# Performance work log

Hardware: AMD Instinct MI355X
Metric: run time of the kernel (lower is better)

The kernel has to match this reference:

```python
import jax, jax.numpy as jnp
import numpy as np

SEQ, SUB, B, V = 32, 16, 512, 258
U = SEQ // SUB
Z, CH, CO, DH = 512, 1024, 512, 1024


def _lstm_cell(x, h, c, Wi, Wh, bi, bh):
    # torch gate order: input, forget, cell, output
    g = x @ Wi + h @ Wh + bi + bh  # [B, 4H]
    i, f, gg, o = jnp.split(g, 4, axis=-1)
    c = jax.nn.sigmoid(f) * c + jax.nn.sigmoid(i) * jnp.tanh(gg)
    h = jax.nn.sigmoid(o) * jnp.tanh(c)
    return h, c


def _lstm2(xs, h1_0, p1, p2):
    # xs: [T,B,in]; h1_0: [B,H] layer-1 initial hidden.
    # Layer-2 hidden and both cell states start at zero (initialize_state in torch code).
    z0 = jnp.zeros_like(h1_0)
    def step(carry, x):
        h1, c1, h2, c2 = carry
        h1, c1 = _lstm_cell(x, h1, c1, *p1)
        h2, c2 = _lstm_cell(h1, h2, c2, *p2)
        return (h1, c1, h2, c2), h2
    _, hs = jax.lax.scan(step, (h1_0, z0, z0, z0), xs)
    return hs  # [T,B,H] top-layer hidden states


def setup_inputs() -> dict:
    key = jax.random.key(0)
    ks = iter(jax.random.split(key, 40))
    def w(shape, s=0.05):
        return jax.random.normal(next(ks), shape, dtype=jnp.float32) * s
    return {
        "z": jax.random.normal(next(ks), (B, Z), dtype=jnp.float32),
        "x": jax.random.uniform(next(ks), (SEQ, B, V), dtype=jnp.float32),
        "conductor_input": w((1, B, V)),
        "ci_W": w((Z, CH)), "ci_b": w((CH,)),
        "cW1i": w((V, 4 * CH)), "cW1h": w((CH, 4 * CH)), "cb1i": w((4 * CH,)), "cb1h": w((4 * CH,)),
        "cW2i": w((CH, 4 * CH)), "cW2h": w((CH, 4 * CH)), "cb2i": w((4 * CH,)), "cb2h": w((4 * CH,)),
        "co_W": w((CH, CO)), "co_b": w((CO,)),
        "di_W": w((CO, DH)), "di_b": w((DH,)),
        "dW1i": w((CO + V, 4 * DH)), "dW1h": w((DH, 4 * DH)), "db1i": w((4 * DH,)), "db1h": w((4 * DH,)),
        "dW2i": w((DH, 4 * DH)), "dW2h": w((DH, 4 * DH)), "db2i": w((4 * DH,)), "db2h": w((4 * DH,)),
        "fc_W": w((DH, V)), "fc_b": w((V,)),
    }


def reference(z, x, conductor_input, ci_W, ci_b, cW1i, cW1h, cb1i, cb1h, cW2i, cW2h, cb2i, cb2h, co_W, co_b, di_W, di_b, dW1i, dW1h, db1i, db1h, dW2i, dW2h, db2i, db2h, fc_W, fc_b):
    # --- conductor: 2-layer LSTM over U steps of a learned constant input ---
    h1 = jnp.tanh(z @ ci_W + ci_b)  # [B,CH] layer-1 init hidden
    cin = jnp.broadcast_to(conductor_input, (U, B, V))
    ch = _lstm2(cin, h1, (cW1i, cW1h, cb1i, cb1h), (cW2i, cW2h, cb2i, cb2h))  # [U,B,CH]
    c = ch @ co_W + co_b  # [U,B,CO]
    # --- decoder (teacher forcing): state resets each sub-sequence, so the U
    # segments of length SUB are independent given c -> vmap over segments ---
    sos = jnp.zeros((1, B, V), jnp.float32).at[:, :, 0].set(1.0)
    prev = jnp.concatenate([sos, x[:-1]], axis=0).reshape(U, SUB, B, V)
    cb = jnp.broadcast_to(c[:, None], (U, SUB, B, CO))
    dec_in = jnp.concatenate([cb, prev], axis=-1)  # [U,SUB,B,CO+V]
    def run_seg(xs, cj):
        h1_0 = jnp.tanh(cj @ di_W + di_b)  # [B,DH]
        return _lstm2(xs, h1_0, (dW1i, dW1h, db1i, db1h), (dW2i, dW2h, db2i, db2h))
    hs = jax.vmap(run_seg)(dec_in, c)  # [U,SUB,B,DH]
    logp = jax.nn.log_softmax(hs @ fc_W + fc_b, axis=-1)  # log(softmax(.)) fused
    return logp.reshape(SEQ, B, V).transpose(1, 0, 2)  # [B,SEQ,V]
```

## Files before the change

kernel.cpp:

```cpp
#include <hip/hip_runtime.h>
#include <cstddef>
#include <cstdint>


namespace {

typedef short s8v __attribute__((ext_vector_type(8)));
typedef float f4v __attribute__((ext_vector_type(4)));
typedef unsigned short ushort_t;

__device__ inline unsigned short f2bf(float f) {
    union { float f; unsigned u; } v; v.f = f;
    unsigned r = v.u + 0x7fff + ((v.u >> 16) & 1);
    return (unsigned short)(r >> 16);
}
__device__ inline float bf2f(ushort_t u) {
    union { unsigned u; float f; } v; v.u = ((unsigned)u) << 16; return v.f;
}

#define GLOAD_LDS(gp, lp)                                              \
    __builtin_amdgcn_global_load_lds(                                  \
        (const __attribute__((address_space(1))) void*)(gp),           \
        (__attribute__((address_space(3))) void*)(lp), 16, 0, 0)

__device__ __forceinline__ void gemm_core(
    const ushort_t* __restrict__ A1a, const ushort_t* __restrict__ A1b,
    int lda1, int K1, const ushort_t* __restrict__ B1t,
    const ushort_t* __restrict__ A2, int lda2, int K2,
    const ushort_t* __restrict__ B2t,
    int bm, int bn, ushort_t* lds, f4v acc[2][4])
{
    const int tid = threadIdx.x;
    const int wid = tid >> 6;
    const int lane = tid & 63;

    const int srow = wid * 16 + (lane >> 2);
    const int rl = srow ^ ((srow >> 2) & 1);
    const int cle = (((lane & 3) ^ (rl & 3)) << 3);

    const int n1 = K1 >> 5;
    const int nt = n1 + (K2 >> 5);

    auto stage = [&](int buf, int t) {
        const ushort_t *Aa, *Ab, *Bt;
        int lda, ldb, k0;
        if (t < n1) { Aa = A1a; Ab = A1b; lda = lda1; Bt = B1t; ldb = K1; k0 = t * 32; }
        else        { Aa = A2; Ab = nullptr; lda = lda2; Bt = B2t; ldb = K2; k0 = (t - n1) * 32; }
        const int grow = bm + rl;
        const ushort_t* ap = (Ab != nullptr && grow >= 512)
                                 ? Ab + (size_t)(grow - 512) * lda + k0 + cle
                                 : Aa + (size_t)grow * lda + k0 + cle;
        GLOAD_LDS(ap, lds + buf * 6144 + wid * 512);
        const ushort_t* bp = Bt + (size_t)(bn + rl) * ldb + k0 + cle;
        GLOAD_LDS(bp, lds + buf * 6144 + 2048 + wid * 512);
        GLOAD_LDS(bp + (size_t)64 * ldb, lds + buf * 6144 + 4096 + wid * 512);
    };

    const int wr = wid >> 1, wc = wid & 1;
    const int lrow = lane & 15, lkg = lane >> 4;

    int aoff[2], boff[4];
#pragma unroll
    for (int m = 0; m < 2; ++m) {
        const int r = wr * 32 + m * 16 + lrow;
        aoff[m] = (r ^ ((r >> 2) & 1)) * 32 + ((lkg ^ (r & 3)) << 3);
    }
#pragma unroll
    for (int n = 0; n < 4; ++n) {
        const int r = wc * 64 + n * 16 + lrow;
        boff[n] = 2048 + (r ^ ((r >> 2) & 1)) * 32 + ((lkg ^ (r & 3)) << 3);
    }

    stage(0, 0);
    __syncthreads();
    int cur = 0;
    for (int t = 0; t < nt; ++t) {
        if (t + 1 < nt) stage(cur ^ 1, t + 1);
        const ushort_t* L = lds + cur * 6144;
        s8v af[2], bfv[4];
#pragma unroll
        for (int m = 0; m < 2; ++m) af[m] = *(const s8v*)(L + aoff[m]);
#pragma unroll
        for (int n = 0; n < 4; ++n) bfv[n] = *(const s8v*)(L + boff[n]);
#pragma unroll
        for (int m = 0; m < 2; ++m)
#pragma unroll
            for (int n = 0; n < 4; ++n)
                acc[m][n] = __builtin_amdgcn_mfma_f32_16x16x32_bf16(
                    af[m], bfv[n], acc[m][n], 0, 0, 0);
        __syncthreads();
        cur ^= 1;
    }
}

template <int ACT>
__global__ __launch_bounds__(256) void plain_gemm(
    const ushort_t* __restrict__ A, int lda, int K,
    const ushort_t* __restrict__ Bt,
    const float* __restrict__ bias, int bias_n,
    float* __restrict__ C, ushort_t* __restrict__ Cbf, int N)
{
    __shared__ __align__(16) ushort_t lds[2 * 6144];
    const int bm = blockIdx.x * 64, bn = blockIdx.y * 128;
    f4v acc[2][4] = {};
    gemm_core(A, nullptr, lda, K, Bt, nullptr, 0, 0, nullptr, bm, bn, lds, acc);

    const int tid = threadIdx.x, wid = tid >> 6, lane = tid & 63;
    const int wr = wid >> 1, wc = wid & 1, lrow = lane & 15, lkg = lane >> 4;
#pragma unroll
    for (int m = 0; m < 2; ++m) {
        const int row0 = bm + wr * 32 + m * 16 + lkg * 4;
#pragma unroll
        for (int n = 0; n < 4; ++n) {
            const int col = bn + wc * 64 + n * 16 + lrow;
            const float bv = (bias != nullptr && col < bias_n) ? bias[col] : 0.f;
#pragma unroll
            for (int r = 0; r < 4; ++r) {
                float v = acc[m][n][r] + bv;
                if (ACT == 1) v = tanhf(v);
                const size_t o = (size_t)(row0 + r) * N + col;
                if (C != nullptr) C[o] = v;
                if (Cbf != nullptr) Cbf[o] = f2bf(v);
            }
        }
    }
}

struct Prob {
    const ushort_t* A1a; const ushort_t* A1b; int lda1; int K1;
    const ushort_t* B1t;
    const ushort_t* A2; int lda2; int K2; const ushort_t* B2t;
    const ushort_t* Dbf;
    const float* bias;
    float* cst;
    ushort_t* hout;
    ushort_t* hs;
    int step_s;
};

__global__ __launch_bounds__(256) void lstm_step(Prob PA, int nxa, Prob PB)
{
    __shared__ __align__(16) ushort_t lds[2 * 6144];
    const int bx = blockIdx.x;
    const bool isA = bx < nxa;
    const Prob& P = isA ? PA : PB;
    const int bm = (isA ? bx : bx - nxa) * 64;
    const int bn = blockIdx.y * 128;

    f4v acc[2][4] = {};
    gemm_core(P.A1a, P.A1b, P.lda1, P.K1, P.B1t,
              P.A2, P.lda2, P.K2, P.B2t, bm, bn, lds, acc);

    const int tid = threadIdx.x, wid = tid >> 6, lane = tid & 63;
    const int wr = wid >> 1, wc = wid & 1, lrow = lane & 15, lkg = lane >> 4;
    const int colbase = bn + wc * 64;
    const int jb = (colbase >> 6) * 16 + lrow;

#pragma unroll
    for (int m = 0; m < 2; ++m) {
        const int row0 = bm + wr * 32 + m * 16 + lkg * 4;
#pragma unroll
        for (int r = 0; r < 4; ++r) {
            const int row = row0 + r;
            float g0 = acc[m][0][r], g1 = acc[m][1][r];
            float g2 = acc[m][2][r], g3 = acc[m][3][r];
            if (P.Dbf != nullptr) {
                const ushort_t* d = P.Dbf + (size_t)row * 4096 + colbase + lrow;
                g0 += bf2f(d[0]); g1 += bf2f(d[16]); g2 += bf2f(d[32]); g3 += bf2f(d[48]);
            }
            if (P.bias != nullptr) {
                const float* b = P.bias + colbase + lrow;
                g0 += b[0]; g1 += b[16]; g2 += b[32]; g3 += b[48];
            }
            const size_t ci = (size_t)row * 1024 + jb;
            const float si = 1.f / (1.f + expf(-g0));
            const float sf = 1.f / (1.f + expf(-g1));
            const float so = 1.f / (1.f + expf(-g3));
            const float cn = fmaf(sf, P.cst[ci], si * tanhf(g2));
            const float hn = so * tanhf(cn);
            P.cst[ci] = cn;
            const ushort_t hb = f2bf(hn);
            P.hout[ci] = hb;
            if (P.hs != nullptr) {
                size_t d;
                if (P.step_s >= 0) {
                    const int u = row >> 9, b = row & 511;
                    d = ((size_t)((u * 16 + P.step_s) * 512 + b) << 10) + jb;
                } else {
                    d = ci;
                }
                P.hs[d] = hb;
            }
        }
    }
}

template <int PERM>
__global__ __launch_bounds__(256) void transpose_to_bf16(
    const float* __restrict__ in, ushort_t* __restrict__ out,
    int K, int N, int Kp, int Np)
{
    __shared__ float tile[32][33];
    const int k0 = blockIdx.x * 32, n0 = blockIdx.y * 32;
    const int tx = threadIdx.x, ty = threadIdx.y;
#pragma unroll
    for (int q = 0; q < 4; ++q) {
        const int k = k0 + ty + 8 * q, n = n0 + tx;
        tile[ty + 8 * q][tx] = (k < K && n < N) ? in[(size_t)k * N + n] : 0.f;
    }
    __syncthreads();
#pragma unroll
    for (int q = 0; q < 4; ++q) {
        const int n = n0 + ty + 8 * q, k = k0 + tx;
        int np = n;
        if (PERM) np = ((n & 1023) >> 4) * 64 + (n >> 10) * 16 + (n & 15);
        out[(size_t)np * Kp + k] = f2bf(tile[tx][ty + 8 * q]);
    }
}

__global__ void convert_pad_bf16(const float* __restrict__ in,
                                 ushort_t* __restrict__ out,
                                 int K, int Kp, int total)
{
    const int idx = blockIdx.x * 256 + threadIdx.x;
    if (idx >= total) return;
    const int r = idx / Kp, k = idx - r * Kp;
    out[idx] = (k < K) ? f2bf(in[(size_t)r * K + k]) : (ushort_t)0;
}

__global__ void sos_init_bf16(ushort_t* __restrict__ sos)
{
    const int i = blockIdx.x * 256 + threadIdx.x;
    if (i < 512 * 288) sos[i] = ((i % 288) == 0) ? (ushort_t)0x3F80 : (ushort_t)0;
}

__global__ void permute_bias(const float* __restrict__ b1,
                             const float* __restrict__ b2,
                             float* __restrict__ out)
{
    const int c = blockIdx.x * 256 + threadIdx.x;
    if (c >= 4096) return;
    const int g = (c >> 4) & 3;
    const int j = (c >> 6) * 16 + (c & 15);
    out[c] = b1[g * 1024 + j] + b2[g * 1024 + j];
}

__global__ __launch_bounds__(256) void logsoftmax_kernel(
    const float* __restrict__ logits, float* __restrict__ out)
{
    const int row = blockIdx.x;
    const int tid = threadIdx.x;
    const float* L = logits + (size_t)row * 384;
    const int t = row >> 9;
    const int b = row & 511;
    float* O = out + ((size_t)b * 32 + t) * 258;

    const float x0 = L[tid];
    const float x1 = (tid < 2) ? L[256 + tid] : -1e30f;

    __shared__ float sm[4];
    float m = fmaxf(x0, x1);
#pragma unroll
    for (int off = 32; off > 0; off >>= 1) m = fmaxf(m, __shfl_down(m, off));
    if ((tid & 63) == 0) sm[tid >> 6] = m;
    __syncthreads();
    m = fmaxf(fmaxf(sm[0], sm[1]), fmaxf(sm[2], sm[3]));
    __syncthreads();

    float s = expf(x0 - m) + ((tid < 2) ? expf(x1 - m) : 0.f);
#pragma unroll
    for (int off = 32; off > 0; off >>= 1) s += __shfl_down(s, off);
    if ((tid & 63) == 0) sm[tid >> 6] = s;
    __syncthreads();
    s = sm[0] + sm[1] + sm[2] + sm[3];

    const float lse = m + logf(s);
    O[tid] = x0 - lse;
    if (tid < 2) O[256 + tid] = x1 - lse;
}

}

extern "C" void kernel_launch(void* const* d_in, const int* in_sizes, int n_in,
                              void* d_out, int out_size, void* d_ws, size_t ws_size,
                              hipStream_t stream)
{
    (void)in_sizes; (void)n_in; (void)out_size; (void)ws_size;

    const float* z    = (const float*)d_in[0];
    const float* x    = (const float*)d_in[1];
    const float* cin  = (const float*)d_in[2];
    const float* ciW  = (const float*)d_in[3];
    const float* cib  = (const float*)d_in[4];
    const float* cW1i = (const float*)d_in[5];
    const float* cW1h = (const float*)d_in[6];
    const float* cb1i = (const float*)d_in[7];
    const float* cb1h = (const float*)d_in[8];
    const float* cW2i = (const float*)d_in[9];
    const float* cW2h = (const float*)d_in[10];
    const float* cb2i = (const float*)d_in[11];
    const float* cb2h = (const float*)d_in[12];
    const float* coW  = (const float*)d_in[13];
    const float* cob  = (const float*)d_in[14];
    const float* diW  = (const float*)d_in[15];
    const float* dib  = (const float*)d_in[16];
    const float* dW1i = (const float*)d_in[17];
    const float* dW1h = (const float*)d_in[18];
    const float* db1i = (const float*)d_in[19];
    const float* db1h = (const float*)d_in[20];
    const float* dW2i = (const float*)d_in[21];
    const float* dW2h = (const float*)d_in[22];
    const float* db2i = (const float*)d_in[23];
    const float* db2h = (const float*)d_in[24];
    const float* fcW  = (const float*)d_in[25];
    const float* fcb  = (const float*)d_in[26];
    float* out = (float*)d_out;

    char* wsp = (char*)d_ws;
    size_t off = 0;
    auto allocf = [&](size_t n) { float* p = (float*)(wsp + off); off += n * 4; return p; };
    auto allocb = [&](size_t n) { ushort_t* p = (ushort_t*)(wsp + off); off += n * 2; return p; };

    float* cst = allocf((size_t)3 * 1024 * 1024 + 64);
    float* c1c = cst;
    float* c2c = cst + (size_t)512 * 1024;
    float* c1d = cst + (size_t)1024 * 1024;
    float* c2d = cst + (size_t)2 * 1024 * 1024;
    float* pb1c = allocf(4096);
    float* pb2c = allocf(4096);
    float* pb1d = allocf(4096);
    float* pb2d = allocf(4096);
    float* logits = allocf((size_t)16384 * 384);

    ushort_t* h2z  = allocb((size_t)2 * (512 + 1024) * 1024);
    ushort_t* hc2A = h2z;
    ushort_t* hc2B = h2z + (size_t)512 * 1024;
    ushort_t* h2dA = h2z + (size_t)2 * 512 * 1024;
    ushort_t* h2dB = h2z + (size_t)(2 * 512 + 1024) * 1024;

    ushort_t* hc1A = allocb((size_t)512 * 1024);
    ushort_t* hc1B = allocb((size_t)512 * 1024);
    ushort_t* h1dA = allocb((size_t)1024 * 1024);
    ushort_t* h1dB = allocb((size_t)1024 * 1024);

    ushort_t* zbf    = allocb((size_t)512 * 512);
    ushort_t* cinbf  = allocb((size_t)512 * 288);
    ushort_t* sosbf  = allocb((size_t)512 * 288);
    ushort_t* xbf    = allocb((size_t)16384 * 288);
    ushort_t* chbf   = allocb((size_t)1024 * 1024);
    ushort_t* ccode  = allocb((size_t)1024 * 512);
    ushort_t* cpre   = allocb((size_t)1024 * 4096);
    ushort_t* xW1c   = allocb((size_t)512 * 4096);
    ushort_t* hsbf   = allocb((size_t)16384 * 1024);

    ushort_t* ciWt  = allocb((size_t)1024 * 512);
    ushort_t* cW1it = allocb((size_t)4096 * 288);
    ushort_t* cW1ht = allocb((size_t)4096 * 1024);
    ushort_t* cW2it = allocb((size_t)4096 * 1024);
    ushort_t* cW2ht = allocb((size_t)4096 * 1024);
    ushort_t* coWt  = allocb((size_t)512 * 1024);
    ushort_t* dtopt = allocb((size_t)4096 * 512);
    ushort_t* dbott = allocb((size_t)4096 * 288);
    ushort_t* diWt  = allocb((size_t)1024 * 512);
    ushort_t* dW1ht = allocb((size_t)4096 * 1024);
    ushort_t* dW2it = allocb((size_t)4096 * 1024);
    ushort_t* dW2ht = allocb((size_t)4096 * 1024);
    ushort_t* fcWt  = allocb((size_t)384 * 1024);

    hipMemsetAsync(cst, 0, (size_t)3 * 1024 * 1024 * 4, stream);
    hipMemsetAsync(h2z, 0, (size_t)2 * (512 + 1024) * 1024 * 2, stream);

    auto transp = [&](const float* in, ushort_t* o, int K, int N, int Kp, int Np, int perm) {
        dim3 g(Kp / 32, Np / 32), b(32, 8);
        if (perm) transpose_to_bf16<1><<<g, b, 0, stream>>>(in, o, K, N, Kp, Np);
        else      transpose_to_bf16<0><<<g, b, 0, stream>>>(in, o, K, N, Kp, Np);
    };
    transp(ciW, ciWt, 512, 1024, 512, 1024, 0);
    transp(cW1i, cW1it, 258, 4096, 288, 4096, 1);
    transp(cW1h, cW1ht, 1024, 4096, 1024, 4096, 1);
    transp(cW2i, cW2it, 1024, 4096, 1024, 4096, 1);
    transp(cW2h, cW2ht, 1024, 4096, 1024, 4096, 1);
    transp(coW, coWt, 1024, 512, 1024, 512, 0);
    transp(dW1i, dtopt, 512, 4096, 512, 4096, 1);
    transp(dW1i + (size_t)512 * 4096, dbott, 258, 4096, 288, 4096, 1);
    transp(diW, diWt, 512, 1024, 512, 1024, 0);
    transp(dW1h, dW1ht, 1024, 4096, 1024, 4096, 1);
    transp(dW2i, dW2it, 1024, 4096, 1024, 4096, 1);
    transp(dW2h, dW2ht, 1024, 4096, 1024, 4096, 1);
    transp(fcW, fcWt, 1024, 258, 1024, 384, 0);

    auto convert = [&](const float* in, ushort_t* o, int K, int Kp, int R) {
        const int total = R * Kp;
        convert_pad_bf16<<<dim3((total + 255) / 256), 256, 0, stream>>>(in, o, K, Kp, total);
    };
    convert(z, zbf, 512, 512, 512);
    convert(cin, cinbf, 258, 288, 512);
    convert(x, xbf, 258, 288, 16384);
    sos_init_bf16<<<dim3((512 * 288 + 255) / 256), 256, 0, stream>>>(sosbf);
    permute_bias<<<16, 256, 0, stream>>>(cb1i, cb1h, pb1c);
    permute_bias<<<16, 256, 0, stream>>>(cb2i, cb2h, pb2c);
    permute_bias<<<16, 256, 0, stream>>>(db1i, db1h, pb1d);
    permute_bias<<<16, 256, 0, stream>>>(db2i, db2h, pb2d);

    auto gemm = [&](int act, const ushort_t* A, int lda, int K, const ushort_t* Bt,
                    const float* bias, int bias_n,
                    float* C, ushort_t* Cbf, int M, int N) {
        dim3 g(M / 64, N / 128);
        if (act) plain_gemm<1><<<g, 256, 0, stream>>>(A, lda, K, Bt, bias, bias_n, C, Cbf, N);
        else     plain_gemm<0><<<g, 256, 0, stream>>>(A, lda, K, Bt, bias, bias_n, C, Cbf, N);
    };

    gemm(1, zbf, 512, 512, ciWt, cib, 1024, nullptr, hc1A, 512, 1024);
    gemm(0, cinbf, 288, 288, cW1it, pb1c, 4096, nullptr, xW1c, 512, 4096);

    ushort_t* HC1[2] = {hc1A, hc1B};
    ushort_t* HC2[2] = {hc2A, hc2B};
    for (int k = 0; k <= 2; ++k) {
        Prob pa{}, pb{};
        int nxa = 0, nxb = 0;
        if (k < 2) {
            pa = {HC1[k & 1], nullptr, 1024, 1024, cW1ht,
                  nullptr, 0, 0, nullptr,
                  xW1c, nullptr, c1c, HC1[(k + 1) & 1], nullptr, -1};
            nxa = 8;
        }
        if (k >= 1) {
            pb = {HC1[k & 1], nullptr, 1024, 1024, cW2it,
                  HC2[k & 1], 1024, 1024, cW2ht,
                  nullptr, pb2c, c2c, HC2[(k + 1) & 1],
                  chbf + (size_t)(k - 1) * 512 * 1024, -1};
            nxb = 8;
        }
        lstm_step<<<dim3(nxa + nxb, 32), 256, 0, stream>>>(pa, nxa, pb);
    }

    gemm(0, chbf, 1024, 1024, coWt, cob, 512, nullptr, ccode, 1024, 512);
    gemm(0, ccode, 512, 512, dtopt, pb1d, 4096, nullptr, cpre, 1024, 4096);
    gemm(1, ccode, 512, 512, diWt, dib, 1024, nullptr, h1dA, 1024, 1024);

    ushort_t* H1[2] = {h1dA, h1dB};
    ushort_t* H2[2] = {h2dA, h2dB};
    for (int k = 0; k <= 16; ++k) {
        Prob pa{}, pb{};
        int nxa = 0, nxb = 0;
        if (k < 16) {
            const ushort_t* plo = (k == 0) ? sosbf : (xbf + (size_t)(k - 1) * 512 * 288);
            const ushort_t* phi = xbf + (size_t)(15 + k) * 512 * 288;
            pa = {plo, phi, 288, 288, dbott,
                  H1[k & 1], 1024, 1024, dW1ht,
                  cpre, nullptr, c1d, H1[(k + 1) & 1], nullptr, -1};
            nxa = 16;
        }
        if (k >= 1) {
            pb = {H1[k & 1], nullptr, 1024, 1024, dW2it,
                  H2[k & 1], 1024, 1024, dW2ht,
                  nullptr, pb2d, c2d, H2[(k + 1) & 1], hsbf, k - 1};
            nxb = 16;
        }
        lstm_step<<<dim3(nxa + nxb, 32), 256, 0, stream>>>(pa, nxa, pb);
    }

    gemm(0, hsbf, 1024, 1024, fcWt, fcb, 258, logits, nullptr, 16384, 384);
    logsoftmax_kernel<<<dim3(16384), 256, 0, stream>>>(logits, out);
}
```

Baseline: 1.365 ms.

## Enlarge GEMM tiles to 128x128, swizzle block order, use fast gate math

Raises the per-block tile in the shared GEMM core from 64x128 to 128x128, so each wave computes a 4x4 MFMA grid and B tiles are reused across twice as many rows. The LSTM step kernel moves to a 1-D grid with an XCD-style swizzle of block IDs, and the staging loop is split into two phases with pointer increments instead of per-step address recomputation. Sigmoid and tanh use __expf-based approximations. The trade-off is half as many blocks per launch, which lowers occupancy and parallelism on a large GPU, plus slightly lower precision in the gate nonlinearities.

```diff
diff --git a/kernel.cpp b/kernel.cpp
--- a/kernel.cpp
+++ b/kernel.cpp
@@ -16,6 +16,11 @@
 }
 __device__ inline float bf2f(ushort_t u) {
     union { unsigned u; float f; } v; v.u = ((unsigned)u) << 16; return v.f;
+}
+__device__ inline float sigm_f(float x) { return 1.f / (1.f + __expf(-x)); }
+__device__ inline float tanh_f(float x) {
+    const float e = __expf(2.f * fabsf(x));
+    return copysignf(1.f - 2.f / (e + 1.f), x);
 }
 
 #define GLOAD_LDS(gp, lp)                                              \
@@ -28,66 +33,89 @@
     int lda1, int K1, const ushort_t* __restrict__ B1t,
     const ushort_t* __restrict__ A2, int lda2, int K2,
     const ushort_t* __restrict__ B2t,
-    int bm, int bn, ushort_t* lds, f4v acc[2][4])
+    int bm, int bn, ushort_t* lds, f4v acc[4][4])
 {
     const int tid = threadIdx.x;
     const int wid = tid >> 6;
     const int lane = tid & 63;
 
-    const int srow = wid * 16 + (lane >> 2);
-    const int rl = srow ^ ((srow >> 2) & 1);
-    const int cle = (((lane & 3) ^ (rl & 3)) << 3);
-
-    const int n1 = K1 >> 5;
-    const int nt = n1 + (K2 >> 5);
-
-    auto stage = [&](int buf, int t) {
-        const ushort_t *Aa, *Ab, *Bt;
-        int lda, ldb, k0;
-        if (t < n1) { Aa = A1a; Ab = A1b; lda = lda1; Bt = B1t; ldb = K1; k0 = t * 32; }
-        else        { Aa = A2; Ab = nullptr; lda = lda2; Bt = B2t; ldb = K2; k0 = (t - n1) * 32; }
-        const int grow = bm + rl;
-        const ushort_t* ap = (Ab != nullptr && grow >= 512)
-                                 ? Ab + (size_t)(grow - 512) * lda + k0 + cle
-                                 : Aa + (size_t)grow * lda + k0 + cle;
-        GLOAD_LDS(ap, lds + buf * 6144 + wid * 512);
-        const ushort_t* bp = Bt + (size_t)(bn + rl) * ldb + k0 + cle;
-        GLOAD_LDS(bp, lds + buf * 6144 + 2048 + wid * 512);
-        GLOAD_LDS(bp + (size_t)64 * ldb, lds + buf * 6144 + 4096 + wid * 512);
+    const int sr0 = wid * 16 + (lane >> 2);
+    const int sr1 = sr0 + 64;
+    const int rl0 = sr0 ^ ((sr0 >> 2) & 1);
+    const int rl1 = sr1 ^ ((sr1 >> 2) & 1);
+    const int c0 = (((lane & 3) ^ (rl0 & 3)) << 3);
+    const int c1 = (((lane & 3) ^ (rl1 & 3)) << 3);
+    const int ldst = wid * 512;
+
+    auto arow = [&](const ushort_t* Aa, const ushort_t* Ab, int lda,
+                    int r) -> const ushort_t* {
+        return (Ab != nullptr && r >= 512) ? Ab + (size_t)(r - 512) * lda
+                                           : Aa + (size_t)r * lda;
+    };
+    const ushort_t* a0 = arow(A1a, A1b, lda1, bm + rl0) + c0;
+    const ushort_t* a1 = arow(A1a, A1b, lda1, bm + rl1) + c1;
+    const ushort_t* b0 = B1t + (size_t)(bn + rl0) * K1 + c0;
+    const ushort_t* b1 = B1t + (size_t)(bn + rl1) * K1 + c1;
+
+    auto stage = [&](int buf) {
+        ushort_t* Lb = lds + buf * 8192;
+        GLOAD_LDS(a0, Lb + ldst);
+        GLOAD_LDS(a1, Lb + 2048 + ldst);
+        GLOAD_LDS(b0, Lb + 4096 + ldst);
+        GLOAD_LDS(b1, Lb + 6144 + ldst);
+        a0 += 32; a1 += 32; b0 += 32; b1 += 32;
     };
 
     const int wr = wid >> 1, wc = wid & 1;
     const int lrow = lane & 15, lkg = lane >> 4;
-
-    int aoff[2], boff[4];
-#pragma unroll
-    for (int m = 0; m < 2; ++m) {
-        const int r = wr * 32 + m * 16 + lrow;
+    int aoff[4], boff[4];
+#pragma unroll
+    for (int m = 0; m < 4; ++m) {
+        const int r = wr * 64 + m * 16 + lrow;
         aoff[m] = (r ^ ((r >> 2) & 1)) * 32 + ((lkg ^ (r & 3)) << 3);
     }
 #pragma unroll
     for (int n = 0; n < 4; ++n) {
         const int r = wc * 64 + n * 16 + lrow;
-        boff[n] = 2048 + (r ^ ((r >> 2) & 1)) * 32 + ((lkg ^ (r & 3)) << 3);
-    }
-
-    stage(0, 0);
+        boff[n] = 4096 + (r ^ ((r >> 2) & 1)) * 32 + ((lkg ^ (r & 3)) << 3);
+    }
+
+    auto compute = [&](int buf) {
+        const ushort_t* L = lds + buf * 8192;
+        s8v af[4], bv[4];
+#pragma unroll
+        for (int m = 0; m < 4; ++m) af[m] = *(const s8v*)(L + aoff[m]);
+#pragma unroll
+        for (int n = 0; n < 4; ++n) bv[n] = *(const s8v*)(L + boff[n]);
+#pragma unroll
+        for (int m = 0; m < 4; ++m)
+#pragma unroll
+            for (int n = 0; n < 4; ++n)
+                acc[m][n] = __builtin_amdgcn_mfma_f32_16x16x32_bf16(
+                    af[m], bv[n], acc[m][n], 0, 0, 0);
+    };
+
+    const int n1 = K1 >> 5, n2 = K2 >> 5;
+    stage(0);
     __syncthreads();
     int cur = 0;
-    for (int t = 0; t < nt; ++t) {
-        if (t + 1 < nt) stage(cur ^ 1, t + 1);
-        const ushort_t* L = lds + cur * 6144;
-        s8v af[2], bfv[4];
-#pragma unroll
-        for (int m = 0; m < 2; ++m) af[m] = *(const s8v*)(L + aoff[m]);
-#pragma unroll
-        for (int n = 0; n < 4; ++n) bfv[n] = *(const s8v*)(L + boff[n]);
-#pragma unroll
-        for (int m = 0; m < 2; ++m)
-#pragma unroll
-            for (int n = 0; n < 4; ++n)
-                acc[m][n] = __builtin_amdgcn_mfma_f32_16x16x32_bf16(
-                    af[m], bfv[n], acc[m][n], 0, 0, 0);
+    for (int t = 0; t < n1; ++t) {
+        if (t + 1 < n1) {
+            stage(cur ^ 1);
+        } else if (n2 > 0) {
+            a0 = A2 + (size_t)(bm + rl0) * lda2 + c0;
+            a1 = A2 + (size_t)(bm + rl1) * lda2 + c1;
+            b0 = B2t + (size_t)(bn + rl0) * K2 + c0;
+            b1 = B2t + (size_t)(bn + rl1) * K2 + c1;
+            stage(cur ^ 1);
+        }
+        compute(cur);
+        __syncthreads();
+        cur ^= 1;
+    }
+    for (int t = 0; t < n2; ++t) {
+        if (t + 1 < n2) stage(cur ^ 1);
+        compute(cur);
         __syncthreads();
         cur ^= 1;
     }
@@ -100,16 +128,16 @@
     const float* __restrict__ bias, int bias_n,
     float* __restrict__ C, ushort_t* __restrict__ Cbf, int N)
 {
-    __shared__ __align__(16) ushort_t lds[2 * 6144];
-    const int bm = blockIdx.x * 64, bn = blockIdx.y * 128;
-    f4v acc[2][4] = {};
+    __shared__ __align__(16) ushort_t lds[2 * 8192];
+    const int bm = blockIdx.x * 128, bn = blockIdx.y * 128;
+    f4v acc[4][4] = {};
     gemm_core(A, nullptr, lda, K, Bt, nullptr, 0, 0, nullptr, bm, bn, lds, acc);
 
     const int tid = threadIdx.x, wid = tid >> 6, lane = tid & 63;
     const int wr = wid >> 1, wc = wid & 1, lrow = lane & 15, lkg = lane >> 4;
 #pragma unroll
-    for (int m = 0; m < 2; ++m) {
-        const int row0 = bm + wr * 32 + m * 16 + lkg * 4;
+    for (int m = 0; m < 4; ++m) {
+        const int row0 = bm + wr * 64 + m * 16 + lkg * 4;
 #pragma unroll
         for (int n = 0; n < 4; ++n) {
             const int col = bn + wc * 64 + n * 16 + lrow;
@@ -117,7 +145,7 @@
 #pragma unroll
             for (int r = 0; r < 4; ++r) {
                 float v = acc[m][n][r] + bv;
-                if (ACT == 1) v = tanhf(v);
+                if (ACT == 1) v = tanh_f(v);
                 const size_t o = (size_t)(row0 + r) * N + col;
                 if (C != nullptr) C[o] = v;
                 if (Cbf != nullptr) Cbf[o] = f2bf(v);
@@ -138,16 +166,23 @@
     int step_s;
 };
 
-__global__ __launch_bounds__(256) void lstm_step(Prob PA, int nxa, Prob PB)
-{
-    __shared__ __align__(16) ushort_t lds[2 * 6144];
-    const int bx = blockIdx.x;
-    const bool isA = bx < nxa;
+__global__ __launch_bounds__(256) void lstm_step(Prob PA, int nxa, Prob PB,
+                                                 int mshift)
+{
+    __shared__ __align__(16) ushort_t lds[2 * 8192];
+    const int nblk = gridDim.x;
+    const int wg = blockIdx.x;
+    const int swz = (wg & 7) * (nblk >> 3) + (wg >> 3);
+    const int nmb = 1 << mshift;
+    const int nb = swz >> mshift;
+    const int mb = swz & (nmb - 1);
+
+    const bool isA = mb < nxa;
     const Prob& P = isA ? PA : PB;
-    const int bm = (isA ? bx : bx - nxa) * 64;
-    const int bn = blockIdx.y * 128;
-
-    f4v acc[2][4] = {};
+    const int bm = (isA ? mb : mb - nxa) * 128;
+    const int bn = nb * 128;
+
+    f4v acc[4][4] = {};
     gemm_core(P.A1a, P.A1b, P.lda1, P.K1, P.B1t,
               P.A2, P.lda2, P.K2, P.B2t, bm, bn, lds, acc);
 
@@ -157,8 +192,8 @@
     const int jb = (colbase >> 6) * 16 + lrow;
 
 #pragma unroll
-    for (int m = 0; m < 2; ++m) {
-        const int row0 = bm + wr * 32 + m * 16 + lkg * 4;
+    for (int m = 0; m < 4; ++m) {
+        const int row0 = bm + wr * 64 + m * 16 + lkg * 4;
 #pragma unroll
         for (int r = 0; r < 4; ++r) {
             const int row = row0 + r;
@@ -166,18 +201,16 @@
             float g2 = acc[m][2][r], g3 = acc[m][3][r];
             if (P.Dbf != nullptr) {
                 const ushort_t* d = P.Dbf + (size_t)row * 4096 + colbase + lrow;
-                g0 += bf2f(d[0]); g1 += bf2f(d[16]); g2 += bf2f(d[32]); g3 += bf2f(d[48]);
+                g0 += bf2f(d[0]); g1 += bf2f(d[16]);
+                g2 += bf2f(d[32]); g3 += bf2f(d[48]);
             }
             if (P.bias != nullptr) {
                 const float* b = P.bias + colbase + lrow;
                 g0 += b[0]; g1 += b[16]; g2 += b[32]; g3 += b[48];
             }
             const size_t ci = (size_t)row * 1024 + jb;
-            const float si = 1.f / (1.f + expf(-g0));
-            const float sf = 1.f / (1.f + expf(-g1));
-            const float so = 1.f / (1.f + expf(-g3));
-            const float cn = fmaf(sf, P.cst[ci], si * tanhf(g2));
-            const float hn = so * tanhf(cn);
+            const float cn = fmaf(sigm_f(g1), P.cst[ci], sigm_f(g0) * tanh_f(g2));
+            const float hn = sigm_f(g3) * tanh_f(cn);
             P.cst[ci] = cn;
             const ushort_t hb = f2bf(hn);
             P.hout[ci] = hb;
@@ -405,7 +438,7 @@
     auto gemm = [&](int act, const ushort_t* A, int lda, int K, const ushort_t* Bt,
                     const float* bias, int bias_n,
                     float* C, ushort_t* Cbf, int M, int N) {
-        dim3 g(M / 64, N / 128);
+        dim3 g(M / 128, N / 128);
         if (act) plain_gemm<1><<<g, 256, 0, stream>>>(A, lda, K, Bt, bias, bias_n, C, Cbf, N);
         else     plain_gemm<0><<<g, 256, 0, stream>>>(A, lda, K, Bt, bias, bias_n, C, Cbf, N);
     };
@@ -422,16 +455,18 @@
             pa = {HC1[k & 1], nullptr, 1024, 1024, cW1ht,
                   nullptr, 0, 0, nullptr,
                   xW1c, nullptr, c1c, HC1[(k + 1) & 1], nullptr, -1};
-            nxa = 8;
+            nxa = 4;
         }
         if (k >= 1) {
             pb = {HC1[k & 1], nullptr, 1024, 1024, cW2it,
                   HC2[k & 1], 1024, 1024, cW2ht,
                   nullptr, pb2c, c2c, HC2[(k + 1) & 1],
                   chbf + (size_t)(k - 1) * 512 * 1024, -1};
-            nxb = 8;
-        }
-        lstm_step<<<dim3(nxa + nxb, 32), 256, 0, stream>>>(pa, nxa, pb);
+            nxb = 4;
+        }
+        const int nmb = nxa + nxb;
+        const int mshift = (nmb == 4) ? 2 : 3;
+        lstm_step<<<dim3(nmb * 32), 256, 0, stream>>>(pa, nxa, pb, mshift);
     }
 
     gemm(0, chbf, 1024, 1024, coWt, cob, 512, nullptr, ccode, 1024, 512);
@@ -449,15 +484,17 @@
             pa = {plo, phi, 288, 288, dbott,
                   H1[k & 1], 1024, 1024, dW1ht,
                   cpre, nullptr, c1d, H1[(k + 1) & 1], nullptr, -1};
-            nxa = 16;
+            nxa = 8;
         }
         if (k >= 1) {
             pb = {H1[k & 1], nullptr, 1024, 1024, dW2it,
                   H2[k & 1], 1024, 1024, dW2ht,
                   nullptr, pb2d, c2d, H2[(k + 1) & 1], hsbf, k - 1};
-            nxb = 16;
-        }
-        lstm_step<<<dim3(nxa + nxb, 32), 256, 0, stream>>>(pa, nxa, pb);
+            nxb = 8;
+        }
+        const int nmb = nxa + nxb;
+        const int mshift = (nmb == 8) ? 3 : 4;
+        lstm_step<<<dim3(nmb * 32), 256, 0, stream>>>(pa, nxa, pb, mshift);
     }
 
     gemm(0, hsbf, 1024, 1024, fcWt, fcb, 258, logits, nullptr, 16384, 384);
```

Result: faster. 1.143 ms (-16.3%).
